# Kernel tuning notes

Measured on AMD Instinct MI355X. Metric: run time of the kernel, lower is better.

## Reference

```python
import jax, jax.numpy as jnp
import numpy as np

NUM_BASES = 8


def setup_inputs() -> dict:
    key = jax.random.key(0)
    ks = jax.random.split(key, 8)
    N, E = 100000, 1600000
    IN_F, OUT_F, NUM_RELS = 128, 128, 16
    si = IN_F // NUM_BASES   # 16
    so = OUT_F // NUM_BASES  # 16
    return {
        "h": jax.random.normal(ks[0], (N, IN_F), dtype=jnp.float32),
        "norm": jax.random.uniform(ks[1], (N, 1), dtype=jnp.float32),
        "edge_src": jax.random.randint(ks[2], (E,), 0, N, dtype=jnp.int32),
        "edge_dst": jax.random.randint(ks[3], (E,), 0, N, dtype=jnp.int32),
        "edge_type": jax.random.randint(ks[4], (E,), 0, NUM_RELS, dtype=jnp.int32),
        "weight": jax.random.normal(ks[5], (NUM_RELS, NUM_BASES * si * so), dtype=jnp.float32) * 0.1,
        "bias_param": jax.random.normal(ks[6], (OUT_F,), dtype=jnp.float32) * 0.1,
        "loop_weight": jax.random.normal(ks[7], (IN_F, OUT_F), dtype=jnp.float32) * 0.1,
    }


def reference(h, norm, edge_src, edge_dst, edge_type, weight, bias_param, loop_weight):
    N, in_feat = h.shape
    out_feat = loop_weight.shape[1]
    si = in_feat // NUM_BASES
    so = out_feat // NUM_BASES
    E = edge_type.shape[0]

    # self-loop message (dropout=0.0 -> identity)
    loop_message = h @ loop_weight                      # [N, out_feat]

    # msg_func: gather per-edge relation weight blocks and do block-diag bmm
    W = weight[edge_type].reshape(E, NUM_BASES, si, so)  # [E, B, si, so]
    src = h[edge_src].reshape(E, NUM_BASES, si)          # [E, B, si]
    msg = jnp.einsum("ebi,ebio->ebo", src, W).reshape(E, out_feat)

    # scatter-sum messages to destination nodes, rescale by norm
    agg = jax.ops.segment_sum(msg, edge_dst, num_segments=N)  # [N, out_feat]
    node_repr = agg * norm

    # bias + self-loop + activation
    node_repr = node_repr + bias_param + loop_message
    return jax.nn.relu(node_repr)
```

## Files before the change

### kernel.cpp

```cpp
#include <hip/hip_runtime.h>


__device__ __forceinline__ unsigned int f2bf(float f) {
  const unsigned int u = __float_as_uint(f);
  return (u + 0x7FFFu + ((u >> 16) & 1u)) >> 16;
}

__global__ __launch_bounds__(256) void rgcn_init_kernel(
    const float* __restrict__ h, const float* __restrict__ loop_w,
    const float* __restrict__ bias, float* __restrict__ out, int N) {
  __shared__ float lw[128 * 128];
  for (int idx = threadIdx.x; idx < 128 * 128 / 4; idx += 256) {
    ((float4*)lw)[idx] = ((const float4*)loop_w)[idx];
  }
  __syncthreads();

  const int lane = threadIdx.x & 63;
  const int wid = threadIdx.x >> 6;
  const int group0 = blockIdx.x * 4 + wid;
  const int ngroups = gridDim.x * 4;
  const int totgroups = (N + 3) >> 2;
  const float b0 = bias[lane];
  const float b1 = bias[64 + lane];

  for (int g = group0; g < totgroups; g += ngroups) {
    const int n0 = g * 4;
    const int nn = (N - n0 < 4) ? (N - n0) : 4;
    if (nn == 4) {
      const float* __restrict__ r0 = h + (size_t)n0 * 128;
      const float* __restrict__ r1 = r0 + 128;
      const float* __restrict__ r2 = r1 + 128;
      const float* __restrict__ r3 = r2 + 128;
      float a00 = b0, a01 = b1, a10 = b0, a11 = b1;
      float a20 = b0, a21 = b1, a30 = b0, a31 = b1;
#pragma unroll 4
      for (int k = 0; k < 128; ++k) {
        const float w0 = lw[k * 128 + lane];
        const float w1 = lw[k * 128 + 64 + lane];
        a00 = fmaf(r0[k], w0, a00); a01 = fmaf(r0[k], w1, a01);
        a10 = fmaf(r1[k], w0, a10); a11 = fmaf(r1[k], w1, a11);
        a20 = fmaf(r2[k], w0, a20); a21 = fmaf(r2[k], w1, a21);
        a30 = fmaf(r3[k], w0, a30); a31 = fmaf(r3[k], w1, a31);
      }
      float* __restrict__ o0 = out + (size_t)n0 * 128;
      o0[lane] = a00;        o0[64 + lane] = a01;
      o0[128 + lane] = a10;  o0[192 + lane] = a11;
      o0[256 + lane] = a20;  o0[320 + lane] = a21;
      o0[384 + lane] = a30;  o0[448 + lane] = a31;
    } else {
      for (int r = 0; r < nn; ++r) {
        const int n = n0 + r;
        const float* __restrict__ hr = h + (size_t)n * 128;
        float a0 = b0, a1 = b1;
#pragma unroll 4
        for (int k = 0; k < 128; ++k) {
          const float a = hr[k];
          a0 = fmaf(a, lw[k * 128 + lane], a0);
          a1 = fmaf(a, lw[k * 128 + 64 + lane], a1);
        }
        out[(size_t)n * 128 + lane] = a0;
        out[(size_t)n * 128 + 64 + lane] = a1;
      }
    }
  }
}

__global__ __launch_bounds__(1024) void rgcn_precompute_kernel(
    const float* __restrict__ h, const float* __restrict__ weight,
    unsigned int* __restrict__ M, int N) {
  const int lane = threadIdx.x & 63;
  const int t = threadIdx.x >> 6;
  const int b = lane >> 4;
  const int o = lane & 15;

  const float* __restrict__ wb = weight + t * 2048 + b * 256 + o;
  float wlo[16], whi[16];
#pragma unroll
  for (int i = 0; i < 16; ++i) {
    wlo[i] = wb[i * 16];
    whi[i] = wb[1024 + i * 16];
  }

  const int n0 = (int)(((long)blockIdx.x * N) / gridDim.x);
  const int n1 = (int)(((long)(blockIdx.x + 1) * N) / gridDim.x);

#pragma unroll 2
  for (int n = n0; n < n1; ++n) {
    const float4* __restrict__ hp =
        (const float4*)(h + (size_t)n * 128) + (b << 2);
    const float4 x0 = hp[0], x1 = hp[1], x2 = hp[2], x3 = hp[3];
    const float4 y0 = hp[16], y1 = hp[17], y2 = hp[18], y3 = hp[19];

    float a0 = x0.x * wlo[0], a1 = x0.y * wlo[1];
    a0 = fmaf(x0.z, wlo[2], a0);  a1 = fmaf(x0.w, wlo[3], a1);
    a0 = fmaf(x1.x, wlo[4], a0);  a1 = fmaf(x1.y, wlo[5], a1);
    a0 = fmaf(x1.z, wlo[6], a0);  a1 = fmaf(x1.w, wlo[7], a1);
    a0 = fmaf(x2.x, wlo[8], a0);  a1 = fmaf(x2.y, wlo[9], a1);
    a0 = fmaf(x2.z, wlo[10], a0); a1 = fmaf(x2.w, wlo[11], a1);
    a0 = fmaf(x3.x, wlo[12], a0); a1 = fmaf(x3.y, wlo[13], a1);
    a0 = fmaf(x3.z, wlo[14], a0); a1 = fmaf(x3.w, wlo[15], a1);

    float c0 = y0.x * whi[0], c1 = y0.y * whi[1];
    c0 = fmaf(y0.z, whi[2], c0);  c1 = fmaf(y0.w, whi[3], c1);
    c0 = fmaf(y1.x, whi[4], c0);  c1 = fmaf(y1.y, whi[5], c1);
    c0 = fmaf(y1.z, whi[6], c0);  c1 = fmaf(y1.w, whi[7], c1);
    c0 = fmaf(y2.x, whi[8], c0);  c1 = fmaf(y2.y, whi[9], c1);
    c0 = fmaf(y2.z, whi[10], c0); c1 = fmaf(y2.w, whi[11], c1);
    c0 = fmaf(y3.x, whi[12], c0); c1 = fmaf(y3.y, whi[13], c1);
    c0 = fmaf(y3.z, whi[14], c0); c1 = fmaf(y3.w, whi[15], c1);

    const unsigned int pk = f2bf(a0 + a1) | (f2bf(c0 + c1) << 16);
    M[(((size_t)n << 4) | t) * 64 + lane] = pk;
  }
}

__global__ __launch_bounds__(256) void rgcn_zero_kernel(int* __restrict__ p,
                                                        int n) {
  for (int i = blockIdx.x * 256 + threadIdx.x; i < n; i += gridDim.x * 256)
    p[i] = 0;
}

__global__ __launch_bounds__(256) void rgcn_hist_kernel(
    const int* __restrict__ edst, int* __restrict__ cnt, int E) {
  for (int e = blockIdx.x * 256 + threadIdx.x; e < E; e += gridDim.x * 256)
    atomicAdd(&cnt[edst[e]], 1);
}

__global__ __launch_bounds__(1024) void rgcn_scan_kernel(
    const int* __restrict__ cnt, int* __restrict__ row_ptr,
    int* __restrict__ cursor, int bins) {
  __shared__ int part[1024];
  const int t = threadIdx.x;
  const int chunk = (bins + 1023) >> 10;
  const int lo = t * chunk;
  const int hi = min(bins, lo + chunk);
  int s = 0;
  for (int i = lo; i < hi; ++i) s += cnt[i];
  part[t] = s;
  __syncthreads();
#pragma unroll
  for (int off = 1; off < 1024; off <<= 1) {
    const int add = (t >= off) ? part[t - off] : 0;
    __syncthreads();
    part[t] += add;
    __syncthreads();
  }
  int run = (t == 0) ? 0 : part[t - 1];
  for (int i = lo; i < hi; ++i) {
    const int c = cnt[i];
    row_ptr[i] = run;
    cursor[i] = run;
    run += c;
  }
  if (t == 1023) row_ptr[bins] = part[1023];
}

__global__ __launch_bounds__(256) void rgcn_scatter_kernel(
    const int* __restrict__ esrc, const int* __restrict__ edst,
    const int* __restrict__ etype, int* __restrict__ cursor,
    int* __restrict__ srec, int E) {
  for (int e = blockIdx.x * 256 + threadIdx.x; e < E; e += gridDim.x * 256) {
    const int d = edst[e];
    const int p = atomicAdd(&cursor[d], 1);
    srec[p] = (esrc[e] << 4) | etype[e];
  }
}

__global__ __launch_bounds__(256) void rgcn_gather3_kernel(
    const float* __restrict__ norm, const int* __restrict__ srec,
    const int* __restrict__ row_ptr, const unsigned int* __restrict__ M,
    float* __restrict__ out, int N) {
  const int lane = threadIdx.x & 63;
  const int d = blockIdx.x * 4 + (threadIdx.x >> 6);
  if (d >= N) return;

  const int e0 = row_ptr[d];
  const int e1 = row_ptr[d + 1];
  float acc0 = 0.f, acc1 = 0.f;

  int e = e0;
  for (; e + 4 <= e1; e += 4) {
    const int r0 = srec[e], r1 = srec[e + 1], r2 = srec[e + 2],
              r3 = srec[e + 3];
    const unsigned int v0 = M[(size_t)r0 * 64 + lane];
    const unsigned int v1 = M[(size_t)r1 * 64 + lane];
    const unsigned int v2 = M[(size_t)r2 * 64 + lane];
    const unsigned int v3 = M[(size_t)r3 * 64 + lane];
    acc0 += __uint_as_float(v0 << 16);
    acc1 += __uint_as_float(v0 & 0xFFFF0000u);
    acc0 += __uint_as_float(v1 << 16);
    acc1 += __uint_as_float(v1 & 0xFFFF0000u);
    acc0 += __uint_as_float(v2 << 16);
    acc1 += __uint_as_float(v2 & 0xFFFF0000u);
    acc0 += __uint_as_float(v3 << 16);
    acc1 += __uint_as_float(v3 & 0xFFFF0000u);
  }
  for (; e < e1; ++e) {
    const unsigned int v = M[(size_t)srec[e] * 64 + lane];
    acc0 += __uint_as_float(v << 16);
    acc1 += __uint_as_float(v & 0xFFFF0000u);
  }

  const float nm = norm[d];
  float* __restrict__ op = out + ((size_t)d << 7);
  op[lane] = fmaxf(fmaf(acc0, nm, op[lane]), 0.f);
  op[64 + lane] = fmaxf(fmaf(acc1, nm, op[64 + lane]), 0.f);
}

__global__ __launch_bounds__(256) void rgcn_edge_kernel(
    const float* __restrict__ h, const float* __restrict__ norm,
    const int* __restrict__ esrc, const int* __restrict__ edst,
    const int* __restrict__ etype, const float* __restrict__ weight,
    float* __restrict__ out, int E) {
  const int lane = threadIdx.x & 63;
  const int wid = threadIdx.x >> 6;
  const int wave0 = blockIdx.x * 4 + wid;
  const int nwaves = gridDim.x * 4;
  const int b = lane >> 4;
  const int o = lane & 15;

  for (int e = wave0; e < E; e += nwaves) {
    const int src = esrc[e];
    const int dst = edst[e];
    const int et = etype[e];
    const float s_lo = h[src * 128 + lane];
    const float s_hi = h[src * 128 + 64 + lane];
    const float nrm = norm[dst];
    const float* __restrict__ Wb = weight + et * 2048 + b * 256 + o;
    float m0 = 0.f, m1 = 0.f;
#pragma unroll
    for (int i = 0; i < 16; ++i) {
      const float a_lo = __shfl(s_lo, (lane & 48) + i, 64);
      const float a_hi = __shfl(s_hi, (lane & 48) + i, 64);
      m0 = fmaf(a_lo, Wb[i * 16], m0);
      m1 = fmaf(a_hi, Wb[1024 + i * 16], m1);
    }
    atomicAdd(&out[dst * 128 + lane], m0 * nrm);
    atomicAdd(&out[dst * 128 + 64 + lane], m1 * nrm);
  }
}

__global__ __launch_bounds__(256) void rgcn_relu_kernel(float* __restrict__ out,
                                                        int total4) {
  int i = blockIdx.x * 256 + threadIdx.x;
  const int stride = gridDim.x * 256;
  for (; i < total4; i += stride) {
    float4 v = ((float4*)out)[i];
    v.x = fmaxf(v.x, 0.f);
    v.y = fmaxf(v.y, 0.f);
    v.z = fmaxf(v.z, 0.f);
    v.w = fmaxf(v.w, 0.f);
    ((float4*)out)[i] = v;
  }
}

extern "C" void kernel_launch(void* const* d_in, const int* in_sizes, int n_in,
                              void* d_out, int out_size, void* d_ws, size_t ws_size,
                              hipStream_t stream) {
  const float* h      = (const float*)d_in[0];
  const float* norm   = (const float*)d_in[1];
  const int*   esrc   = (const int*)d_in[2];
  const int*   edst   = (const int*)d_in[3];
  const int*   etype  = (const int*)d_in[4];
  const float* weight = (const float*)d_in[5];
  const float* bias   = (const float*)d_in[6];
  const float* loop_w = (const float*)d_in[7];
  float* out = (float*)d_out;

  const int N = in_sizes[0] / 128;
  const int E = in_sizes[2];
  const int nrels = in_sizes[5] / 2048;

  rgcn_init_kernel<<<2048, 256, 0, stream>>>(h, loop_w, bias, out, N);

  const size_t ofs_cnt = 0;
  const size_t ofs_rp = ofs_cnt + (size_t)N;
  const size_t ofs_cur = (ofs_rp + N + 1 + 3) & ~(size_t)3;
  const size_t ofs_srec = (ofs_cur + N + 3) & ~(size_t)3;
  const size_t ofs_M = (ofs_srec + E + 15) & ~(size_t)15;
  const size_t need = (ofs_M + ((size_t)N << 4) * 64) * 4;

  if (nrels == 16 && N < (1 << 26) && ws_size >= need) {
    int* base    = (int*)d_ws;
    int* cnt     = base + ofs_cnt;
    int* row_ptr = base + ofs_rp;
    int* cursor  = base + ofs_cur;
    int* srec    = base + ofs_srec;
    unsigned int* M = (unsigned int*)(base + ofs_M);

    rgcn_precompute_kernel<<<512, 1024, 0, stream>>>(h, weight, M, N);
    rgcn_zero_kernel<<<128, 256, 0, stream>>>(cnt, N);
    rgcn_hist_kernel<<<2048, 256, 0, stream>>>(edst, cnt, E);
    rgcn_scan_kernel<<<1, 1024, 0, stream>>>(cnt, row_ptr, cursor, N);
    rgcn_scatter_kernel<<<2048, 256, 0, stream>>>(esrc, edst, etype, cursor,
                                                  srec, E);
    rgcn_gather3_kernel<<<(N + 3) / 4, 256, 0, stream>>>(norm, srec, row_ptr,
                                                         M, out, N);
  } else {
    rgcn_edge_kernel<<<4096, 256, 0, stream>>>(h, norm, esrc, edst, etype,
                                               weight, out, E);
    rgcn_relu_kernel<<<2048, 256, 0, stream>>>(out, (N * 128) / 4);
  }
}
```

Baseline: 928.8 us.

## Partition source nodes into chunks so the per-source message table stays cache-resident

Edges are bucketed by (source chunk, destination) so the aggregation can run in passes. Each pass precomputes the bf16 per-relation message table only for the current source window and gathers only those edges. Destinations with no edges are skipped on non-final passes, and ReLU is applied only in the last pass. The aim is to keep the gathered table small enough for the caches, at the cost of more histogram bins, more kernel launches and repeated read-modify-write of the output. The chunk size search starts at 2^17, which is larger than N here, so a single chunk is likely chosen; the precompute grid is also halved.

```diff
diff --git a/kernel.cpp b/kernel.cpp
--- a/kernel.cpp
+++ b/kernel.cpp
@@ -67,7 +67,7 @@
 
 __global__ __launch_bounds__(1024) void rgcn_precompute_kernel(
     const float* __restrict__ h, const float* __restrict__ weight,
-    unsigned int* __restrict__ M, int N) {
+    unsigned int* __restrict__ M, int base, int cend) {
   const int lane = threadIdx.x & 63;
   const int t = threadIdx.x >> 6;
   const int b = lane >> 4;
@@ -81,8 +81,9 @@
     whi[i] = wb[1024 + i * 16];
   }
 
-  const int n0 = (int)(((long)blockIdx.x * N) / gridDim.x);
-  const int n1 = (int)(((long)(blockIdx.x + 1) * N) / gridDim.x);
+  const int span = cend - base;
+  const int n0 = base + (int)(((long)blockIdx.x * span) / gridDim.x);
+  const int n1 = base + (int)(((long)(blockIdx.x + 1) * span) / gridDim.x);
 
 #pragma unroll 2
   for (int n = n0; n < n1; ++n) {
@@ -110,7 +111,7 @@
     c0 = fmaf(y3.z, whi[14], c0); c1 = fmaf(y3.w, whi[15], c1);
 
     const unsigned int pk = f2bf(a0 + a1) | (f2bf(c0 + c1) << 16);
-    M[(((size_t)n << 4) | t) * 64 + lane] = pk;
+    M[(((size_t)(n - base) << 4) | t) * 64 + lane] = pk;
   }
 }
 
@@ -121,9 +122,12 @@
 }
 
 __global__ __launch_bounds__(256) void rgcn_hist_kernel(
-    const int* __restrict__ edst, int* __restrict__ cnt, int E) {
-  for (int e = blockIdx.x * 256 + threadIdx.x; e < E; e += gridDim.x * 256)
-    atomicAdd(&cnt[edst[e]], 1);
+    const int* __restrict__ esrc, const int* __restrict__ edst,
+    int* __restrict__ cnt, int E, int N, int logS) {
+  for (int e = blockIdx.x * 256 + threadIdx.x; e < E; e += gridDim.x * 256) {
+    const int key = (int)(((unsigned)esrc[e] >> logS) * (unsigned)N) + edst[e];
+    atomicAdd(&cnt[key], 1);
+  }
 }
 
 __global__ __launch_bounds__(1024) void rgcn_scan_kernel(
@@ -135,6 +139,7 @@
   const int lo = t * chunk;
   const int hi = min(bins, lo + chunk);
   int s = 0;
+#pragma unroll 4
   for (int i = lo; i < hi; ++i) s += cnt[i];
   part[t] = s;
   __syncthreads();
@@ -158,26 +163,29 @@
 __global__ __launch_bounds__(256) void rgcn_scatter_kernel(
     const int* __restrict__ esrc, const int* __restrict__ edst,
     const int* __restrict__ etype, int* __restrict__ cursor,
-    int* __restrict__ srec, int E) {
+    int* __restrict__ srec, int E, int N, int logS) {
+  const int mask = (1 << logS) - 1;
   for (int e = blockIdx.x * 256 + threadIdx.x; e < E; e += gridDim.x * 256) {
-    const int d = edst[e];
-    const int p = atomicAdd(&cursor[d], 1);
-    srec[p] = (esrc[e] << 4) | etype[e];
+    const int s = esrc[e];
+    const int key = (int)(((unsigned)s >> logS) * (unsigned)N) + edst[e];
+    const int p = atomicAdd(&cursor[key], 1);
+    srec[p] = ((s & mask) << 4) | etype[e];
   }
 }
 
 __global__ __launch_bounds__(256) void rgcn_gather3_kernel(
     const float* __restrict__ norm, const int* __restrict__ srec,
-    const int* __restrict__ row_ptr, const unsigned int* __restrict__ M,
-    float* __restrict__ out, int N) {
+    const int* __restrict__ rpc, const unsigned int* __restrict__ M,
+    float* __restrict__ out, int N, int final_pass) {
   const int lane = threadIdx.x & 63;
   const int d = blockIdx.x * 4 + (threadIdx.x >> 6);
   if (d >= N) return;
 
-  const int e0 = row_ptr[d];
-  const int e1 = row_ptr[d + 1];
+  const int e0 = rpc[d];
+  const int e1 = rpc[d + 1];
+  if (!final_pass && e0 == e1) return;
+
   float acc0 = 0.f, acc1 = 0.f;
-
   int e = e0;
   for (; e + 4 <= e1; e += 4) {
     const int r0 = srec[e], r1 = srec[e + 1], r2 = srec[e + 2],
@@ -203,8 +211,14 @@
 
   const float nm = norm[d];
   float* __restrict__ op = out + ((size_t)d << 7);
-  op[lane] = fmaxf(fmaf(acc0, nm, op[lane]), 0.f);
-  op[64 + lane] = fmaxf(fmaf(acc1, nm, op[64 + lane]), 0.f);
+  float v0 = fmaf(acc0, nm, op[lane]);
+  float v1 = fmaf(acc1, nm, op[64 + lane]);
+  if (final_pass) {
+    v0 = fmaxf(v0, 0.f);
+    v1 = fmaxf(v1, 0.f);
+  }
+  op[lane] = v0;
+  op[64 + lane] = v1;
 }
 
 __global__ __launch_bounds__(256) void rgcn_edge_kernel(
@@ -273,29 +287,52 @@
 
   rgcn_init_kernel<<<2048, 256, 0, stream>>>(h, loop_w, bias, out, N);
 
-  const size_t ofs_cnt = 0;
-  const size_t ofs_rp = ofs_cnt + (size_t)N;
-  const size_t ofs_cur = (ofs_rp + N + 1 + 3) & ~(size_t)3;
-  const size_t ofs_srec = (ofs_cur + N + 3) & ~(size_t)3;
-  const size_t ofs_M = (ofs_srec + E + 15) & ~(size_t)15;
-  const size_t need = (ofs_M + ((size_t)N << 4) * 64) * 4;
-
-  if (nrels == 16 && N < (1 << 26) && ws_size >= need) {
+  int chosenK = -1, C = 1;
+  size_t ofs_rp = 0, ofs_cur = 0, ofs_srec = 0, ofs_M = 0;
+  if (nrels == 16 && N >= 1 && N < (1 << 26)) {
+    for (int k = 17; k >= 12; --k) {
+      const int S = 1 << k;
+      const int cc = (N + S - 1) >> k;
+      const size_t bins = (size_t)cc * (size_t)N;
+      if (bins > (size_t)1 << 27) continue;
+      const size_t mrows = ((size_t)(S < N ? S : N)) << 4;
+      const size_t o_rp = bins;
+      const size_t o_cur = (o_rp + bins + 1 + 3) & ~(size_t)3;
+      const size_t o_srec = (o_cur + bins + 3) & ~(size_t)3;
+      const size_t o_M = (o_srec + (size_t)E + 15) & ~(size_t)15;
+      const size_t need = (o_M + mrows * 64) * 4;
+      if (need <= ws_size) {
+        chosenK = k; C = cc;
+        ofs_rp = o_rp; ofs_cur = o_cur; ofs_srec = o_srec; ofs_M = o_M;
+        break;
+      }
+    }
+  }
+
+  if (chosenK >= 0) {
+    const int S = 1 << chosenK;
+    const int bins = C * N;
     int* base    = (int*)d_ws;
-    int* cnt     = base + ofs_cnt;
+    int* cnt     = base;
     int* row_ptr = base + ofs_rp;
     int* cursor  = base + ofs_cur;
     int* srec    = base + ofs_srec;
     unsigned int* M = (unsigned int*)(base + ofs_M);
 
-    rgcn_precompute_kernel<<<512, 1024, 0, stream>>>(h, weight, M, N);
-    rgcn_zero_kernel<<<128, 256, 0, stream>>>(cnt, N);
-    rgcn_hist_kernel<<<2048, 256, 0, stream>>>(edst, cnt, E);
-    rgcn_scan_kernel<<<1, 1024, 0, stream>>>(cnt, row_ptr, cursor, N);
+    rgcn_zero_kernel<<<256, 256, 0, stream>>>(cnt, bins);
+    rgcn_hist_kernel<<<2048, 256, 0, stream>>>(esrc, edst, cnt, E, N, chosenK);
+    rgcn_scan_kernel<<<1, 1024, 0, stream>>>(cnt, row_ptr, cursor, bins);
     rgcn_scatter_kernel<<<2048, 256, 0, stream>>>(esrc, edst, etype, cursor,
-                                                  srec, E);
-    rgcn_gather3_kernel<<<(N + 3) / 4, 256, 0, stream>>>(norm, srec, row_ptr,
-                                                         M, out, N);
+                                                  srec, E, N, chosenK);
+    for (int c = 0; c < C; ++c) {
+      const int cbase = c << chosenK;
+      const int cend = (cbase + S < N) ? (cbase + S) : N;
+      rgcn_precompute_kernel<<<256, 1024, 0, stream>>>(h, weight, M, cbase,
+                                                       cend);
+      rgcn_gather3_kernel<<<(N + 3) / 4, 256, 0, stream>>>(
+          norm, srec, row_ptr + (size_t)c * N, M, out, N,
+          (c == C - 1) ? 1 : 0);
+    }
   } else {
     rgcn_edge_kernel<<<4096, 256, 0, stream>>>(h, norm, esrc, edst, etype,
                                                weight, out, E);
```

New measurement: 1.746 ms. 1.88x slower.
